# Kernel tuning notes

Measured on AMD Instinct MI355X. Metric: run time of the kernel, lower is better.

The kernel has to match this reference:

```python
import jax, jax.numpy as jnp
import numpy as np
from jax import lax

H, W = 2048, 2048  # output_size


def setup_inputs() -> dict:
    key = jax.random.key(0)
    # normalized [ymin, xmin, ymax, xmax] in [0,1]; invalid (min>=max) boxes are
    # naturally skipped by the empty-mask logic, same as the torch `continue`.
    boxes = jax.random.uniform(key, (1024, 4), dtype=jnp.float32)
    return {"boxes": boxes}


def reference(boxes):
    ys = jnp.arange(H, dtype=jnp.int32)  # [H]
    xs = jnp.arange(W, dtype=jnp.int32)  # [W]

    def paint(smap, box):
        # pixel coords: truncate toward zero like torch .long(), then clamp
        y1 = jnp.maximum(0, (box[0] * H).astype(jnp.int32))
        x1 = jnp.maximum(0, (box[1] * W).astype(jnp.int32))
        y2 = jnp.minimum(H, (box[2] * H).astype(jnp.int32))
        x2 = jnp.minimum(W, (box[3] * W).astype(jnp.int32))
        cover = ((ys >= y1) & (ys < y2))[:, None] & ((xs >= x1) & (xs < x2))[None, :]  # [H,W]
        # channel values: [1.0, ymin, xmin, ymax, xmax] (normalized box coords)
        vals = jnp.concatenate([jnp.ones((1,), boxes.dtype), box])  # [5]
        # later boxes overwrite earlier ones inside their rectangle (paint order)
        new_map = jnp.where(cover[None, :, :], vals[:, None, None], smap)
        return new_map, None

    smap0 = jnp.zeros((5, H, W), dtype=boxes.dtype)
    smap, _ = lax.scan(paint, smap0, boxes)
    return smap[None]  # (1, 5, H, W)
```

## Files before the change

### kernel.cpp

```cpp
#include <hip/hip_runtime.h>

#define HH 2048
#define WW 2048
#define NB 1024
#define TW 128
#define TH 32

__global__ __launch_bounds__(256, 4) void paint_kernel(const float4* __restrict__ boxes,
                                                       float* __restrict__ out) {
    __shared__ unsigned long long imaskS[4][4];
    __shared__ unsigned long long fmaskS[4][4];
    __shared__ uint2 clist[NB];
    __shared__ short cidxS[NB];

    const int tid  = threadIdx.x;
    const int lane = tid & 63;
    const int wid  = tid >> 6;
    const int tileX = blockIdx.x * TW;
    const int tileY = blockIdx.y * TH;

    int ry1[4], rx1[4], ry2[4], rx2[4];
    bool rint[4];
    #pragma unroll
    for (int c = 0; c < 4; ++c) {
        float4 bx = boxes[c * 256 + tid];
        int y1 = max(0, (int)(bx.x * (float)HH));
        int x1 = max(0, (int)(bx.y * (float)WW));
        int y2 = min(HH, (int)(bx.z * (float)HH));
        int x2 = min(WW, (int)(bx.w * (float)WW));
        ry1[c] = y1; rx1[c] = x1; ry2[c] = y2; rx2[c] = x2;
        bool valid = (y1 < y2) && (x1 < x2);
        bool inter = valid && (y1 < tileY + TH) && (y2 > tileY) &&
                     (x1 < tileX + TW) && (x2 > tileX);
        bool full  = (y1 <= tileY) && (y2 >= tileY + TH) &&
                     (x1 <= tileX) && (x2 >= tileX + TW);
        rint[c] = inter;
        unsigned long long mi = __ballot(inter);
        unsigned long long mf = __ballot(full);
        if (lane == 0) { imaskS[c][wid] = mi; fmaskS[c][wid] = mf; }
    }
    __syncthreads();

    int lastFull = -1;
    #pragma unroll
    for (int c = 3; c >= 0; --c)
        #pragma unroll
        for (int w = 3; w >= 0; --w)
            if (lastFull < 0) {
                unsigned long long m = fmaskS[c][w];
                if (m) lastFull = c * 256 + w * 64 + 63 - __clzll(m);
            }

    int cnt_all = 0;
    int myoff[4];
    #pragma unroll
    for (int c = 0; c < 4; ++c) {
        #pragma unroll
        for (int w = 0; w < 4; ++w) {
            unsigned long long m = imaskS[c][w];
            int d = lastFull - (c * 256 + w * 64);
            if (d >= 63) m = 0;
            else if (d >= 0) m &= (~0ull) << (d + 1);
            if (w == wid)
                myoff[c] = cnt_all + __popcll(m & ((1ull << lane) - 1ull));
            cnt_all += __popcll(m);
        }
    }

    #pragma unroll
    for (int c = 0; c < 4; ++c) {
        int b = c * 256 + tid;
        if (rint[c] && b > lastFull) {
            clist[myoff[c]] = make_uint2(((unsigned)ry1[c] << 16) | (unsigned)rx1[c],
                                         ((unsigned)ry2[c] << 16) | (unsigned)rx2[c]);
            cidxS[myoff[c]] = (short)b;
        }
    }
    __syncthreads();

    const int qx  = tid & 31;
    const int px0 = tileX + qx * 4;
    const int ry  = tid >> 5;
    const int py0 = tileY + ry * 4;

    if (cnt_all == 0) {
        float4 bv = make_float4(0.f, 0.f, 0.f, 0.f);
        float on = 0.f;
        if (lastFull >= 0) { bv = boxes[lastFull]; on = 1.f; }
        float vals[5] = {on, bv.x, bv.y, bv.z, bv.w};
        #pragma unroll
        for (int ch = 0; ch < 5; ++ch) {
            float4 v = make_float4(vals[ch], vals[ch], vals[ch], vals[ch]);
            size_t base = (size_t)ch * (HH * WW);
            #pragma unroll
            for (int s = 0; s < 4; ++s)
                *(float4*)(out + base + (size_t)(py0 + s) * WW + px0) = v;
        }
    } else {
        int fnd[4][4];
        #pragma unroll
        for (int s = 0; s < 4; ++s)
            #pragma unroll
            for (int k = 0; k < 4; ++k) fnd[s][k] = lastFull;
        for (int j = 0; j < cnt_all; ++j) {
            uint2 pc = clist[j];
            int bidx = cidxS[j];
            int by1 = (int)(pc.x >> 16), bx1 = (int)(pc.x & 0xffff);
            int by2 = (int)(pc.y >> 16), bx2 = (int)(pc.y & 0xffff);
            #pragma unroll
            for (int s = 0; s < 4; ++s) {
                int py = py0 + s;
                bool yin = (py >= by1) && (py < by2);
                #pragma unroll
                for (int k = 0; k < 4; ++k) {
                    int px = px0 + k;
                    if (yin && px >= bx1 && px < bx2) fnd[s][k] = bidx;
                }
            }
        }
        #pragma unroll
        for (int s = 0; s < 4; ++s) {
            float4 v[5];
            #pragma unroll
            for (int k = 0; k < 4; ++k) {
                int f = fnd[s][k];
                float4 bv = (f >= 0) ? boxes[f] : make_float4(0.f, 0.f, 0.f, 0.f);
                float on = (f >= 0) ? 1.f : 0.f;
                ((float*)&v[0])[k] = on;
                ((float*)&v[1])[k] = bv.x;
                ((float*)&v[2])[k] = bv.y;
                ((float*)&v[3])[k] = bv.z;
                ((float*)&v[4])[k] = bv.w;
            }
            size_t pb = (size_t)(py0 + s) * WW + px0;
            #pragma unroll
            for (int ch = 0; ch < 5; ++ch)
                *(float4*)(out + (size_t)ch * (HH * WW) + pb) = v[ch];
        }
    }
}

extern "C" void kernel_launch(void* const* d_in, const int* in_sizes, int n_in,
                              void* d_out, int out_size, void* d_ws, size_t ws_size,
                              hipStream_t stream) {
    const float4* boxes = (const float4*)d_in[0];
    float* out = (float*)d_out;
    dim3 grid(WW / TW, HH / TH);
    dim3 block(256);
    paint_kernel<<<grid, block, 0, stream>>>(boxes, out);
}
```

Baseline: 91.58 us.

## Restructure into full-row bands with per-strip candidate lists

Each block now handles an 8-row band across the full width instead of a 128x32 tile, so the 1024 boxes are loaded and classified once per band rather than once per tile. Per-strip (128-column) intersect and full-cover masks are built with ballots, and one thread per strip compacts up to 64 candidates, falling back to scanning all boxes past the last full cover when that cap is exceeded. Writes are full-row coalesced float4 stores, with a uniform-value fast path. The cost is more ballots, a serial compaction by 16 threads, and a slow fallback path when strips are crowded.

```diff
diff --git a/kernel.cpp b/kernel.cpp
--- a/kernel.cpp
+++ b/kernel.cpp
@@ -3,139 +3,153 @@
 #define HH 2048
 #define WW 2048
 #define NB 1024
-#define TW 128
-#define TH 32
+#define NT 512
+#define BANDH 8
+#define NSTRIP 16
+#define SW 128
+#define CAP 64
 
-__global__ __launch_bounds__(256, 4) void paint_kernel(const float4* __restrict__ boxes,
-                                                       float* __restrict__ out) {
-    __shared__ unsigned long long imaskS[4][4];
-    __shared__ unsigned long long fmaskS[4][4];
-    __shared__ uint2 clist[NB];
-    __shared__ short cidxS[NB];
+
+__global__ __launch_bounds__(NT, 2) void paint_kernel(const float4* __restrict__ boxes,
+                                                      float* __restrict__ out) {
+    __shared__ uint2 coordS[NB];
+    __shared__ unsigned long long fmS[NSTRIP][2][8];
+    __shared__ unsigned long long imS[NSTRIP][2][8];
+    __shared__ uint2 clistS[NSTRIP][CAP];
+    __shared__ short cidxS[NSTRIP][CAP];
+    __shared__ int lastFullS[NSTRIP];
+    __shared__ int cntS[NSTRIP];
 
     const int tid  = threadIdx.x;
     const int lane = tid & 63;
     const int wid  = tid >> 6;
-    const int tileX = blockIdx.x * TW;
-    const int tileY = blockIdx.y * TH;
+    const int band  = ((blockIdx.x & 7) << 5) | (blockIdx.x >> 3);
+    const int tileY = band * BANDH;
 
-    int ry1[4], rx1[4], ry2[4], rx2[4];
-    bool rint[4];
+    unsigned im16[2], fm16[2];
     #pragma unroll
-    for (int c = 0; c < 4; ++c) {
-        float4 bx = boxes[c * 256 + tid];
+    for (int c = 0; c < 2; ++c) {
+        float4 bx = boxes[c * NT + tid];
         int y1 = max(0, (int)(bx.x * (float)HH));
         int x1 = max(0, (int)(bx.y * (float)WW));
         int y2 = min(HH, (int)(bx.z * (float)HH));
         int x2 = min(WW, (int)(bx.w * (float)WW));
-        ry1[c] = y1; rx1[c] = x1; ry2[c] = y2; rx2[c] = x2;
+        coordS[c * NT + tid] = make_uint2(((unsigned)y1 << 16) | (unsigned)x1,
+                                          ((unsigned)y2 << 16) | (unsigned)x2);
         bool valid = (y1 < y2) && (x1 < x2);
-        bool inter = valid && (y1 < tileY + TH) && (y2 > tileY) &&
-                     (x1 < tileX + TW) && (x2 > tileX);
-        bool full  = (y1 <= tileY) && (y2 >= tileY + TH) &&
-                     (x1 <= tileX) && (x2 >= tileX + TW);
-        rint[c] = inter;
-        unsigned long long mi = __ballot(inter);
-        unsigned long long mf = __ballot(full);
-        if (lane == 0) { imaskS[c][wid] = mi; fmaskS[c][wid] = mf; }
+        bool yint  = valid && (y1 < tileY + BANDH) && (y2 > tileY);
+        bool yfull = valid && (y1 <= tileY) && (y2 >= tileY + BANDH);
+        int ilo = x1 >> 7, ihi = min(NSTRIP, (x2 + SW - 1) >> 7);
+        unsigned imask = 0;
+        if (yint && ihi > ilo) imask = (unsigned)(((1u << (ihi - ilo)) - 1u) << ilo);
+        int clo = (x1 + SW - 1) >> 7, chi = x2 >> 7;
+        unsigned cmask = 0;
+        if (yfull && chi > clo) cmask = (unsigned)(((1u << (chi - clo)) - 1u) << clo);
+        im16[c] = imask; fm16[c] = cmask;
+    }
+    #pragma unroll
+    for (int c = 0; c < 2; ++c)
+        #pragma unroll
+        for (int s = 0; s < NSTRIP; ++s) {
+            unsigned long long bi = __ballot((im16[c] >> s) & 1);
+            unsigned long long bf = __ballot((fm16[c] >> s) & 1);
+            if (lane == 0) { imS[s][c][wid] = bi; fmS[s][c][wid] = bf; }
+        }
+    __syncthreads();
+
+    if (tid < NSTRIP) {
+        const int s = tid;
+        int lf = -1;
+        for (int c = 1; c >= 0 && lf < 0; --c)
+            for (int w = 7; w >= 0 && lf < 0; --w) {
+                unsigned long long m = fmS[s][c][w];
+                if (m) lf = c * 512 + w * 64 + 63 - __clzll(m);
+            }
+        lastFullS[s] = lf;
+        int j = 0;
+        for (int c = 0; c < 2; ++c)
+            for (int w = 0; w < 8; ++w) {
+                unsigned long long m = imS[s][c][w];
+                int base = c * 512 + w * 64;
+                int d = lf - base;
+                if (d >= 63) m = 0;
+                else if (d >= 0) m &= (~0ull) << (d + 1);
+                while (m) {
+                    int b = base + __builtin_ctzll(m);
+                    m &= m - 1;
+                    if (j < CAP) { clistS[s][j] = coordS[b]; cidxS[s][j] = (short)b; }
+                    ++j;
+                }
+            }
+        cntS[s] = (j <= CAP) ? j : -1;
     }
     __syncthreads();
 
-    int lastFull = -1;
+    const int py = tileY + wid;
+    const int lx = lane << 2;
+    int fnd[8][4];
+    bool uni[8];
     #pragma unroll
-    for (int c = 3; c >= 0; --c)
-        #pragma unroll
-        for (int w = 3; w >= 0; --w)
-            if (lastFull < 0) {
-                unsigned long long m = fmaskS[c][w];
-                if (m) lastFull = c * 256 + w * 64 + 63 - __clzll(m);
+    for (int xi = 0; xi < 8; ++xi) {
+        const int s   = xi * 2 + (lane >> 5);
+        const int px0 = xi * 256 + lx;
+        const int lf  = lastFullS[s];
+        int f0 = lf, f1 = lf, f2 = lf, f3 = lf;
+        const int c = cntS[s];
+        if (c >= 0) {
+            for (int j = 0; j < c; ++j) {
+                uint2 pc = clistS[s][j];
+                int bidx = cidxS[s][j];
+                int by1 = (int)(pc.x >> 16), bx1 = (int)(pc.x & 0xffffu);
+                int by2 = (int)(pc.y >> 16), bx2 = (int)(pc.y & 0xffffu);
+                if (py >= by1 && py < by2) {
+                    if (px0     >= bx1 && px0     < bx2) f0 = bidx;
+                    if (px0 + 1 >= bx1 && px0 + 1 < bx2) f1 = bidx;
+                    if (px0 + 2 >= bx1 && px0 + 2 < bx2) f2 = bidx;
+                    if (px0 + 3 >= bx1 && px0 + 3 < bx2) f3 = bidx;
+                }
             }
-
-    int cnt_all = 0;
-    int myoff[4];
-    #pragma unroll
-    for (int c = 0; c < 4; ++c) {
-        #pragma unroll
-        for (int w = 0; w < 4; ++w) {
-            unsigned long long m = imaskS[c][w];
-            int d = lastFull - (c * 256 + w * 64);
-            if (d >= 63) m = 0;
-            else if (d >= 0) m &= (~0ull) << (d + 1);
-            if (w == wid)
-                myoff[c] = cnt_all + __popcll(m & ((1ull << lane) - 1ull));
-            cnt_all += __popcll(m);
-        }
-    }
-
-    #pragma unroll
-    for (int c = 0; c < 4; ++c) {
-        int b = c * 256 + tid;
-        if (rint[c] && b > lastFull) {
-            clist[myoff[c]] = make_uint2(((unsigned)ry1[c] << 16) | (unsigned)rx1[c],
-                                         ((unsigned)ry2[c] << 16) | (unsigned)rx2[c]);
-            cidxS[myoff[c]] = (short)b;
-        }
-    }
-    __syncthreads();
-
-    const int qx  = tid & 31;
-    const int px0 = tileX + qx * 4;
-    const int ry  = tid >> 5;
-    const int py0 = tileY + ry * 4;
-
-    if (cnt_all == 0) {
-        float4 bv = make_float4(0.f, 0.f, 0.f, 0.f);
-        float on = 0.f;
-        if (lastFull >= 0) { bv = boxes[lastFull]; on = 1.f; }
-        float vals[5] = {on, bv.x, bv.y, bv.z, bv.w};
-        #pragma unroll
-        for (int ch = 0; ch < 5; ++ch) {
-            float4 v = make_float4(vals[ch], vals[ch], vals[ch], vals[ch]);
-            size_t base = (size_t)ch * (HH * WW);
-            #pragma unroll
-            for (int s = 0; s < 4; ++s)
-                *(float4*)(out + base + (size_t)(py0 + s) * WW + px0) = v;
-        }
-    } else {
-        int fnd[4][4];
-        #pragma unroll
-        for (int s = 0; s < 4; ++s)
-            #pragma unroll
-            for (int k = 0; k < 4; ++k) fnd[s][k] = lastFull;
-        for (int j = 0; j < cnt_all; ++j) {
-            uint2 pc = clist[j];
-            int bidx = cidxS[j];
-            int by1 = (int)(pc.x >> 16), bx1 = (int)(pc.x & 0xffff);
-            int by2 = (int)(pc.y >> 16), bx2 = (int)(pc.y & 0xffff);
-            #pragma unroll
-            for (int s = 0; s < 4; ++s) {
-                int py = py0 + s;
-                bool yin = (py >= by1) && (py < by2);
-                #pragma unroll
-                for (int k = 0; k < 4; ++k) {
-                    int px = px0 + k;
-                    if (yin && px >= bx1 && px < bx2) fnd[s][k] = bidx;
+        } else {
+            for (int b = lf + 1; b < NB; ++b) {
+                uint2 pc = coordS[b];
+                int by1 = (int)(pc.x >> 16), bx1 = (int)(pc.x & 0xffffu);
+                int by2 = (int)(pc.y >> 16), bx2 = (int)(pc.y & 0xffffu);
+                if (py >= by1 && py < by2) {
+                    if (px0     >= bx1 && px0     < bx2) f0 = b;
+                    if (px0 + 1 >= bx1 && px0 + 1 < bx2) f1 = b;
+                    if (px0 + 2 >= bx1 && px0 + 2 < bx2) f2 = b;
+                    if (px0 + 3 >= bx1 && px0 + 3 < bx2) f3 = b;
                 }
             }
         }
+        fnd[xi][0] = f0; fnd[xi][1] = f1; fnd[xi][2] = f2; fnd[xi][3] = f3;
+        uni[xi] = (f0 == f1) && (f1 == f2) && (f2 == f3);
+    }
+
+    const float* bfp = (const float*)boxes;
+    #pragma unroll
+    for (int ch = 0; ch < 5; ++ch) {
+        float* op = out + (size_t)ch * ((size_t)HH * WW) + (size_t)py * WW;
         #pragma unroll
-        for (int s = 0; s < 4; ++s) {
-            float4 v[5];
-            #pragma unroll
-            for (int k = 0; k < 4; ++k) {
-                int f = fnd[s][k];
-                float4 bv = (f >= 0) ? boxes[f] : make_float4(0.f, 0.f, 0.f, 0.f);
-                float on = (f >= 0) ? 1.f : 0.f;
-                ((float*)&v[0])[k] = on;
-                ((float*)&v[1])[k] = bv.x;
-                ((float*)&v[2])[k] = bv.y;
-                ((float*)&v[3])[k] = bv.z;
-                ((float*)&v[4])[k] = bv.w;
+        for (int xi = 0; xi < 8; ++xi) {
+            float4 v;
+            if (uni[xi]) {
+                int f = fnd[xi][0];
+                float val;
+                if (ch == 0) val = (f >= 0) ? 1.f : 0.f;
+                else         val = (f >= 0) ? bfp[f * 4 + (ch - 1)] : 0.f;
+                v = make_float4(val, val, val, val);
+            } else {
+                #pragma unroll
+                for (int k = 0; k < 4; ++k) {
+                    int f = fnd[xi][k];
+                    float val;
+                    if (ch == 0) val = (f >= 0) ? 1.f : 0.f;
+                    else         val = (f >= 0) ? bfp[f * 4 + (ch - 1)] : 0.f;
+                    ((float*)&v)[k] = val;
+                }
             }
-            size_t pb = (size_t)(py0 + s) * WW + px0;
-            #pragma unroll
-            for (int ch = 0; ch < 5; ++ch)
-                *(float4*)(out + (size_t)ch * (HH * WW) + pb) = v[ch];
+            *(float4*)(op + xi * 256 + lx) = v;
         }
     }
 }
@@ -145,7 +159,7 @@
                               hipStream_t stream) {
     const float4* boxes = (const float4*)d_in[0];
     float* out = (float*)d_out;
-    dim3 grid(WW / TW, HH / TH);
-    dim3 block(256);
+    dim3 grid(HH / BANDH);
+    dim3 block(NT);
     paint_kernel<<<grid, block, 0, stream>>>(boxes, out);
 }
```

Result: slower. 102.1 us (+11.5%).
